# Optimization experiments

Hardware: AMD Instinct MI355X
Metric: run time of the kernel (lower is better)

Reference implementation:

```python
import jax, jax.numpy as jnp
import numpy as np
from jax import lax

K = 3  # ksize (odd)


def _box_mean(x):
    """Edge-clipped k x k mean filter over the last two dims of [B,C,H,W].
    Equivalent to the torch Mean_Filter: sum over the window intersected
    with the image, divided by the actual number of in-bounds pixels."""
    H, W = x.shape[2], x.shape[3]
    sums = lax.reduce_window(x, 0.0, lax.add,
                             window_dimensions=(1, 1, K, K),
                             window_strides=(1, 1, 1, 1),
                             padding='SAME')
    counts = lax.reduce_window(jnp.ones((H, W), x.dtype), 0.0, lax.add,
                               window_dimensions=(K, K),
                               window_strides=(1, 1),
                               padding='SAME')  # [H,W] in-bounds counts
    return sums / counts[None, None, :, :]


def setup_inputs() -> dict:
    key = jax.random.key(0)
    k1, k2, k3 = jax.random.split(key, 3)
    B, C, H, W = 32, 64, 128, 128
    x = jax.random.normal(k1, (B, C, H, W), dtype=jnp.float32)
    # 1x1 conv weight [out_c, in_c] and bias, as in nn.Conv2d(64, 64, 1)
    conv_w = jax.random.normal(k2, (C, C), dtype=jnp.float32) * (1.0 / np.sqrt(C))
    conv_b = jax.random.normal(k3, (C,), dtype=jnp.float32) * 0.01
    return {"x": x, "conv_w": conv_w, "conv_b": conv_b}


def reference(x, conv_w, conv_b):
    # denoising_box forward: x + conv1x1(mean_filter(x))
    x_denoised = _box_mean(x)
    y = jnp.einsum('bchw,oc->bohw', x_denoised, conv_w) + conv_b[None, :, None, None]
    return x + y
```

## Files before the change

### kernel.cpp

```cpp
#include <hip/hip_runtime.h>

#define B_   32
#define C_   64
#define H_   128
#define W_   128
#define HW_  (H_ * W_)
#define CHW_ (C_ * HW_)
#define TH_  4

__global__ __launch_bounds__(256, 3) void denoise_fused(
    const float* __restrict__ x, const float* __restrict__ cw,
    const float* __restrict__ cb, float* __restrict__ out)
{
    __shared__ float xd[C_ * W_];
    __shared__ float Wt[C_ * C_];

    const int t    = threadIdx.x;
    const int b    = blockIdx.x >> 5;
    const int h0   = (blockIdx.x & 31) * TH_;
    const int lane = t & 63;
    const int wid  = t >> 6;
    const int j    = lane & 31;
    const int half = lane >> 5;

    for (int i = t; i < C_ * C_; i += 256) {
        int o = i >> 6, c = i & 63;
        xd[o * 65 + c] = cw[i];
    }
    __syncthreads();
    for (int i = t; i < C_ * C_; i += 256) {
        int c = i >> 6, o = i & 63;
        Wt[i] = xd[o * 65 + c];
    }
    __syncthreads();

    const float* xb = x   + (size_t)b * CHW_;
    float*       ob = out + (size_t)b * CHW_;

    const int o0 = wid * 16 + half * 8;
    float bias[8];
    #pragma unroll
    for (int oi = 0; oi < 8; ++oi) bias[oi] = cb[o0 + oi];

    for (int r = 0; r < TH_; ++r) {
        const int h = h0 + r;
        const bool hm = (h > 0), hp = (h < H_ - 1);
        const float rv = 1.f + (hm ? 1.f : 0.f) + (hp ? 1.f : 0.f);
        const float i3 = 1.f / (rv * 3.f);
        const float i2 = 1.f / (rv * 2.f);

        #pragma unroll
        for (int p = 0; p < 8; ++p) {
            const int c = p * 8 + wid * 2 + half;
            const float* rc = xb + c * HW_ + h * W_;
            float4 v = ((const float4*)rc)[j];
            if (hm) { float4 a = ((const float4*)(rc - W_))[j]; v.x += a.x; v.y += a.y; v.z += a.z; v.w += a.w; }
            if (hp) { float4 a = ((const float4*)(rc + W_))[j]; v.x += a.x; v.y += a.y; v.z += a.z; v.w += a.w; }
            float L = __shfl_up(v.w, 1);
            float R = __shfl_down(v.x, 1);
            float4 d;
            d.x = (j == 0)  ? (v.x + v.y) * i2 : (L + v.x + v.y) * i3;
            d.y = (v.x + v.y + v.z) * i3;
            d.z = (v.y + v.z + v.w) * i3;
            d.w = (j == 31) ? (v.z + v.w) * i2 : (v.z + v.w + R) * i3;
            ((float4*)xd)[c * 32 + j] = d;
        }
        __syncthreads();

        float acc[8][4];
        #pragma unroll
        for (int oi = 0; oi < 8; ++oi)
            acc[oi][0] = acc[oi][1] = acc[oi][2] = acc[oi][3] = 0.f;

        #pragma unroll 4
        for (int c = 0; c < C_; ++c) {
            float4 xv = ((const float4*)xd)[c * 32 + j];
            float4 wa = *(const float4*)&Wt[c * 64 + o0];
            float4 wb = *(const float4*)&Wt[c * 64 + o0 + 4];
            float w8[8] = { wa.x, wa.y, wa.z, wa.w, wb.x, wb.y, wb.z, wb.w };
            #pragma unroll
            for (int oi = 0; oi < 8; ++oi) {
                acc[oi][0] += w8[oi] * xv.x;
                acc[oi][1] += w8[oi] * xv.y;
                acc[oi][2] += w8[oi] * xv.z;
                acc[oi][3] += w8[oi] * xv.w;
            }
        }

        #pragma unroll
        for (int oi = 0; oi < 8; ++oi) {
            const int o = o0 + oi;
            float4 xr = ((const float4*)(xb + o * HW_ + h * W_))[j];
            float4 res;
            res.x = xr.x + acc[oi][0] + bias[oi];
            res.y = xr.y + acc[oi][1] + bias[oi];
            res.z = xr.z + acc[oi][2] + bias[oi];
            res.w = xr.w + acc[oi][3] + bias[oi];
            ((float4*)(ob + o * HW_ + h * W_))[j] = res;
        }
        __syncthreads();
    }
}

extern "C" void kernel_launch(void* const* d_in, const int* in_sizes, int n_in,
                              void* d_out, int out_size, void* d_ws, size_t ws_size,
                              hipStream_t stream) {
    const float* x  = (const float*)d_in[0];
    const float* cw = (const float*)d_in[1];
    const float* cb = (const float*)d_in[2];
    float* out = (float*)d_out;
    dim3 grid(B_ * (H_ / TH_));
    dim3 block(256);
    hipLaunchKernelGGL(denoise_fused, grid, block, 0, stream, x, cw, cb, out);
}
```

Measured before the change: 311.5 us.

## Split rows into column halves and reuse center loads for residual

Each row is now processed in two 64-column halves, so the shared tile and per-thread accumulator footprint shrink. Channel-to-thread mapping is changed so the center pixel loaded for the box filter is the same one needed for the residual, removing the second global read of x. Boundary columns between halves are passed through a small shared buffer, and occupancy hint rises from 3 to 4 blocks. The cost is twice as many barriers per row and extra scalar loads at the split boundary.

```diff
diff --git a/kernel.cpp b/kernel.cpp
--- a/kernel.cpp
+++ b/kernel.cpp
@@ -7,40 +7,43 @@
 #define HW_  (H_ * W_)
 #define CHW_ (C_ * HW_)
 #define TH_  4
+#define CW_  64
 
-__global__ __launch_bounds__(256, 3) void denoise_fused(
+__global__ __launch_bounds__(256, 4) void denoise_fused(
     const float* __restrict__ x, const float* __restrict__ cw,
     const float* __restrict__ cb, float* __restrict__ out)
 {
-    __shared__ float xd[C_ * W_];
-    __shared__ float Wt[C_ * C_];
+    __shared__ __align__(16) float xd[C_ * CW_];
+    __shared__ __align__(16) float Wt[C_ * C_];
+    __shared__ float bnd[C_];
 
     const int t    = threadIdx.x;
     const int b    = blockIdx.x >> 5;
     const int h0   = (blockIdx.x & 31) * TH_;
     const int lane = t & 63;
     const int wid  = t >> 6;
-    const int j    = lane & 31;
-    const int half = lane >> 5;
+    const int jj   = lane & 15;
+    const int sub  = lane >> 4;
+    const int m    = wid * 4 + sub;
 
     for (int i = t; i < C_ * C_; i += 256) {
         int o = i >> 6, c = i & 63;
-        xd[o * 65 + c] = cw[i];
+        xd[o * 64 + ((c + o) & 63)] = cw[i];
     }
     __syncthreads();
-    for (int i = t; i < C_ * C_; i += 256) {
-        int c = i >> 6, o = i & 63;
-        Wt[i] = xd[o * 65 + c];
+    for (int k = t; k < C_ * C_; k += 256) {
+        int c = k >> 6, r = k & 63;
+        int o = (r >> 2) + ((r & 3) << 4);
+        Wt[k] = xd[o * 64 + ((c + o) & 63)];
     }
     __syncthreads();
 
     const float* xb = x   + (size_t)b * CHW_;
     float*       ob = out + (size_t)b * CHW_;
 
-    const int o0 = wid * 16 + half * 8;
-    float bias[8];
+    float bias[4];
     #pragma unroll
-    for (int oi = 0; oi < 8; ++oi) bias[oi] = cb[o0 + oi];
+    for (int oi = 0; oi < 4; ++oi) bias[oi] = cb[m + 16 * oi];
 
     for (int r = 0; r < TH_; ++r) {
         const int h = h0 + r;
@@ -50,55 +53,73 @@
         const float i2 = 1.f / (rv * 2.f);
 
         #pragma unroll
-        for (int p = 0; p < 8; ++p) {
-            const int c = p * 8 + wid * 2 + half;
-            const float* rc = xb + c * HW_ + h * W_;
-            float4 v = ((const float4*)rc)[j];
-            if (hm) { float4 a = ((const float4*)(rc - W_))[j]; v.x += a.x; v.y += a.y; v.z += a.z; v.w += a.w; }
-            if (hp) { float4 a = ((const float4*)(rc + W_))[j]; v.x += a.x; v.y += a.y; v.z += a.z; v.w += a.w; }
-            float L = __shfl_up(v.w, 1);
-            float R = __shfl_down(v.x, 1);
-            float4 d;
-            d.x = (j == 0)  ? (v.x + v.y) * i2 : (L + v.x + v.y) * i3;
-            d.y = (v.x + v.y + v.z) * i3;
-            d.z = (v.y + v.z + v.w) * i3;
-            d.w = (j == 31) ? (v.z + v.w) * i2 : (v.z + v.w + R) * i3;
-            ((float4*)xd)[c * 32 + j] = d;
+        for (int q = 0; q < 2; ++q) {
+            float s[4][4];
+
+            #pragma unroll
+            for (int p = 0; p < 4; ++p) {
+                const int c = 16 * p + m;
+                const float* rc = xb + c * HW_ + h * W_ + q * CW_;
+                float4 cen = ((const float4*)rc)[jj];
+                s[p][0] = cen.x; s[p][1] = cen.y; s[p][2] = cen.z; s[p][3] = cen.w;
+                float4 v = cen;
+                if (hm) { float4 a = ((const float4*)(rc - W_))[jj]; v.x += a.x; v.y += a.y; v.z += a.z; v.w += a.w; }
+                if (hp) { float4 a = ((const float4*)(rc + W_))[jj]; v.x += a.x; v.y += a.y; v.z += a.z; v.w += a.w; }
+                float L = __shfl_up(v.w, 1);
+                float R = __shfl_down(v.x, 1);
+                if (q == 0) {
+                    if (jj == 15) {
+                        bnd[c] = v.w;
+                        const float* rb = rc + CW_;
+                        float vr = rb[0];
+                        if (hm) vr += rb[-W_];
+                        if (hp) vr += rb[W_];
+                        R = vr;
+                    }
+                } else {
+                    if (jj == 0) L = bnd[c];
+                }
+                float4 d;
+                d.x = (q == 0 && jj == 0)  ? (v.x + v.y) * i2 : (L + v.x + v.y) * i3;
+                d.y = (v.x + v.y + v.z) * i3;
+                d.z = (v.y + v.z + v.w) * i3;
+                d.w = (q == 1 && jj == 15) ? (v.z + v.w) * i2 : (v.z + v.w + R) * i3;
+                ((float4*)xd)[c * 16 + jj] = d;
+            }
+            __syncthreads();
+
+            float acc[4][4];
+            #pragma unroll
+            for (int oi = 0; oi < 4; ++oi) {
+                acc[oi][0] = s[oi][0] + bias[oi];
+                acc[oi][1] = s[oi][1] + bias[oi];
+                acc[oi][2] = s[oi][2] + bias[oi];
+                acc[oi][3] = s[oi][3] + bias[oi];
+            }
+
+            #pragma unroll 4
+            for (int c = 0; c < C_; ++c) {
+                float4 xv = ((const float4*)xd)[c * 16 + jj];
+                float4 wv = *(const float4*)&Wt[c * 64 + m * 4];
+                float w4[4] = { wv.x, wv.y, wv.z, wv.w };
+                #pragma unroll
+                for (int oi = 0; oi < 4; ++oi) {
+                    acc[oi][0] += w4[oi] * xv.x;
+                    acc[oi][1] += w4[oi] * xv.y;
+                    acc[oi][2] += w4[oi] * xv.z;
+                    acc[oi][3] += w4[oi] * xv.w;
+                }
+            }
+
+            #pragma unroll
+            for (int oi = 0; oi < 4; ++oi) {
+                float4 res;
+                res.x = acc[oi][0]; res.y = acc[oi][1];
+                res.z = acc[oi][2]; res.w = acc[oi][3];
+                ((float4*)(ob + (m + 16 * oi) * HW_ + h * W_ + q * CW_))[jj] = res;
+            }
+            __syncthreads();
         }
-        __syncthreads();
-
-        float acc[8][4];
-        #pragma unroll
-        for (int oi = 0; oi < 8; ++oi)
-            acc[oi][0] = acc[oi][1] = acc[oi][2] = acc[oi][3] = 0.f;
-
-        #pragma unroll 4
-        for (int c = 0; c < C_; ++c) {
-            float4 xv = ((const float4*)xd)[c * 32 + j];
-            float4 wa = *(const float4*)&Wt[c * 64 + o0];
-            float4 wb = *(const float4*)&Wt[c * 64 + o0 + 4];
-            float w8[8] = { wa.x, wa.y, wa.z, wa.w, wb.x, wb.y, wb.z, wb.w };
-            #pragma unroll
-            for (int oi = 0; oi < 8; ++oi) {
-                acc[oi][0] += w8[oi] * xv.x;
-                acc[oi][1] += w8[oi] * xv.y;
-                acc[oi][2] += w8[oi] * xv.z;
-                acc[oi][3] += w8[oi] * xv.w;
-            }
-        }
-
-        #pragma unroll
-        for (int oi = 0; oi < 8; ++oi) {
-            const int o = o0 + oi;
-            float4 xr = ((const float4*)(xb + o * HW_ + h * W_))[j];
-            float4 res;
-            res.x = xr.x + acc[oi][0] + bias[oi];
-            res.y = xr.y + acc[oi][1] + bias[oi];
-            res.z = xr.z + acc[oi][2] + bias[oi];
-            res.w = xr.w + acc[oi][3] + bias[oi];
-            ((float4*)(ob + o * HW_ + h * W_))[j] = res;
-        }
-        __syncthreads();
     }
 }
 
```

New measurement: 305.2 us. 2.0% less time.
